# Optimization experiments

Measured on AMD Instinct MI355X. Metric: run time of the kernel, lower is better.

The kernel has to match this reference:

```python
import jax, jax.numpy as jnp
import numpy as np

# pywt db4 analysis filters (dec_lo, dec_hi), length 8
DEC_LO = np.array([-0.010597401784997278, 0.032883011666982945, 0.030841381835986965,
                   -0.18703481171888114, -0.02798376941698385, 0.6308807679295904,
                   0.7148465705525415, 0.23037781330885523], dtype=np.float32)
DEC_HI = np.array([-0.23037781330885523, 0.7148465705525415, -0.6308807679295904,
                   -0.02798376941698385, 0.18703481171888114, 0.030841381835986965,
                   -0.032883011666982945, -0.010597401784997278], dtype=np.float32)


def setup_inputs() -> dict:
    key = jax.random.key(0)
    x = jax.random.normal(key, (32, 3, 512, 512), dtype=jnp.float32)
    dec = jnp.stack([jnp.asarray(DEC_LO), jnp.asarray(DEC_HI)])  # (2, 8)
    return {"x": x, "dec": dec}


def _afb1d_last(x, dec):
    """Analysis filter bank along last axis: circular pad (end), stride-2
    cross-correlation with lo/hi filters. x: (..., L) -> (lo, hi) each (..., L//2)."""
    L = x.shape[-1]
    taps = dec.shape[-1]
    pad = taps - 1
    xp = jnp.concatenate([x, x[..., :pad]], axis=-1)          # circular pad at end
    flat = xp.reshape(-1, 1, xp.shape[-1])                    # (N, 1, L+pad)
    out = jax.lax.conv_general_dilated(
        flat, dec[:, None, :], window_strides=(2,), padding='VALID',
        dimension_numbers=('NCH', 'OIH', 'NCH'))              # (N, 2, L//2)
    out = out.reshape(*x.shape[:-1], 2, L // 2)
    return out[..., 0, :], out[..., 1, :]


def reference(x, dec):
    B, C, H, W = x.shape
    xr = x.reshape(B * C, H, W)
    # row pass (along W)
    lo_w, hi_w = _afb1d_last(xr, dec)                         # (BC, H, W//2)
    # column pass (along H): move H to last axis
    lo_t = jnp.swapaxes(lo_w, -2, -1)                         # (BC, W//2, H)
    hi_t = jnp.swapaxes(hi_w, -2, -1)
    ll, lh = _afb1d_last(lo_t, dec)                           # (BC, W//2, H//2)
    hl, hh = _afb1d_last(hi_t, dec)
    coeffs = jnp.stack([ll, lh, hl, hh], axis=1)              # (BC, 4, W//2, H//2)
    coeffs = jnp.swapaxes(coeffs, -2, -1)                     # (BC, 4, H//2, W//2)
    return coeffs.reshape(B, C * 4, H // 2, W // 2)
```

## Files before the change

### kernel.cpp

```cpp
#include <hip/hip_runtime.h>


#define TI 4
#define TJ 64
#define PR (2*TI + 6)
#define HH 512
#define WW 512

__global__ __launch_bounds__(256)
void dwt2d_db4_kernel(const float* __restrict__ x,
                      const float* __restrict__ dec,
                      float* __restrict__ out) {
    __shared__ __align__(16) float sm_lo[PR][TJ];
    __shared__ __align__(16) float sm_hi[PR][TJ];

    const int tid = threadIdx.x;

    const int n  = blockIdx.x;
    const int m  = n >> 3;
    const int jt = m & 3;
    const int it = (n & 7) * 8 + ((m >> 2) & 7);
    const int bc = m >> 5;

    const int rowBase = it * (2 * TI);
    const int colBase = jt * (2 * TJ);

    float flo[8], fhi[8];
#pragma unroll
    for (int k = 0; k < 8; ++k) { flo[k] = dec[k]; fhi[k] = dec[8 + k]; }

    const float* xb = x + (size_t)bc * HH * WW;

    for (int task = tid; task < PR * (TJ / 2); task += 256) {
        int r = task >> 5;
        int t = task & 31;
        int gr = rowBase + r;          if (gr >= HH) gr -= HH;
        int c0 = colBase + 4 * t;
        int c1 = c0 + 4;               if (c1 >= WW) c1 -= WW;
        int c2 = c0 + 8;               if (c2 >= WW) c2 -= WW;
        const float* xr = xb + gr * WW;
        float4 v0 = *(const float4*)(xr + c0);
        float4 v1 = *(const float4*)(xr + c1);
        float4 v2 = *(const float4*)(xr + c2);
        float w[12] = { v0.x, v0.y, v0.z, v0.w,
                        v1.x, v1.y, v1.z, v1.w,
                        v2.x, v2.y, v2.z, v2.w };
        float lo0 = 0.f, hi0 = 0.f, lo1 = 0.f, hi1 = 0.f;
#pragma unroll
        for (int q = 0; q < 8; ++q) {
            lo0 += w[q]     * flo[q];
            hi0 += w[q]     * fhi[q];
            lo1 += w[q + 2] * flo[q];
            hi1 += w[q + 2] * fhi[q];
        }
        *(float2*)&sm_lo[r][2 * t] = make_float2(lo0, lo1);
        *(float2*)&sm_hi[r][2 * t] = make_float2(hi0, hi1);
    }
    __syncthreads();

    {
        int i = tid >> 6;
        int j = tid & 63;
        float ll = 0.f, lh = 0.f, hl = 0.f, hh = 0.f;
#pragma unroll
        for (int p = 0; p < 8; ++p) {
            float a = sm_lo[2 * i + p][j];
            float b = sm_hi[2 * i + p][j];
            float cl = flo[p], ch = fhi[p];
            ll += a * cl; lh += a * ch;
            hl += b * cl; hh += b * ch;
        }
        int oi = it * TI + i;
        int oj = jt * TJ + j;
        size_t base = ((size_t)(bc * 4) * 256 + oi) * 256 + oj;
        __builtin_nontemporal_store(ll, &out[base]);
        __builtin_nontemporal_store(lh, &out[base + 1 * 65536]);
        __builtin_nontemporal_store(hl, &out[base + 2 * 65536]);
        __builtin_nontemporal_store(hh, &out[base + 3 * 65536]);
    }
}

extern "C" void kernel_launch(void* const* d_in, const int* in_sizes, int n_in,
                              void* d_out, int out_size, void* d_ws, size_t ws_size,
                              hipStream_t stream) {
    const float* x   = (const float*)d_in[0];
    const float* dec = (const float*)d_in[1];
    float* out = (float*)d_out;

    dim3 grid(4 * 64 * 96);
    dim3 block(256);
    dwt2d_db4_kernel<<<grid, block, 0, stream>>>(x, dec, out);
}
```

Measured before the change: 176.3 us.

## Replace shared-memory two-pass DWT with per-thread register column streaming

Result: slower. 196.6 us (+11.5%).

```diff
diff --git a/kernel.cpp b/kernel.cpp
--- a/kernel.cpp
+++ b/kernel.cpp
@@ -1,29 +1,74 @@
 #include <hip/hip_runtime.h>
 
 
-#define TI 4
-#define TJ 64
+#define TI 8
 #define PR (2*TI + 6)
 #define HH 512
 #define WW 512
+
+typedef float float4u __attribute__((ext_vector_type(4), aligned(8)));
+typedef float float2u __attribute__((ext_vector_type(2), aligned(8)));
+
+template <bool CWRAP>
+__device__ __forceinline__ void dwt_col(const float* __restrict__ xb,
+                                        int rowBase, int c0,
+                                        const float* flo, const float* fhi,
+                                        float* ll, float* lh, float* hl, float* hh) {
+#pragma unroll
+    for (int r = 0; r < PR; ++r) {
+        int gr = rowBase + r;
+        if (gr >= HH) gr -= HH;
+        const float* xr = xb + gr * WW;
+        float wv[8];
+        if constexpr (!CWRAP) {
+            float4u a = *(const float4u*)(xr + c0);
+            float4u b = *(const float4u*)(xr + c0 + 4);
+            wv[0] = a.x; wv[1] = a.y; wv[2] = a.z; wv[3] = a.w;
+            wv[4] = b.x; wv[5] = b.y; wv[6] = b.z; wv[7] = b.w;
+        } else {
+#pragma unroll
+            for (int k = 0; k < 4; ++k) {
+                int c = c0 + 2 * k;
+                if (c >= WW) c -= WW;
+                float2u v = *(const float2u*)(xr + c);
+                wv[2 * k]     = v.x;
+                wv[2 * k + 1] = v.y;
+            }
+        }
+        float rlo = 0.f, rhi = 0.f;
+#pragma unroll
+        for (int q = 0; q < 8; ++q) { rlo += wv[q] * flo[q]; rhi += wv[q] * fhi[q]; }
+#pragma unroll
+        for (int p = (r & 1); p < 8; p += 2) {
+            int d = r - p;
+            if (d >= 0 && d < 2 * TI) {
+                int i = d >> 1;
+                float cl = flo[p], ch = fhi[p];
+                ll[i] += rlo * cl; lh[i] += rlo * ch;
+                hl[i] += rhi * cl; hh[i] += rhi * ch;
+            }
+        }
+    }
+}
 
 __global__ __launch_bounds__(256)
 void dwt2d_db4_kernel(const float* __restrict__ x,
                       const float* __restrict__ dec,
                       float* __restrict__ out) {
-    __shared__ __align__(16) float sm_lo[PR][TJ];
-    __shared__ __align__(16) float sm_hi[PR][TJ];
+    const int tid  = threadIdx.x;
+    const int lane = tid & 63;
+    const int w    = tid >> 6;
 
-    const int tid = threadIdx.x;
+    const int n   = blockIdx.x;
+    const int itb = n & 7;
+    const int m   = n >> 3;
+    const int jt  = m & 3;
+    const int bc  = m >> 2;
 
-    const int n  = blockIdx.x;
-    const int m  = n >> 3;
-    const int jt = m & 3;
-    const int it = (n & 7) * 8 + ((m >> 2) & 7);
-    const int bc = m >> 5;
-
+    const int it = itb * 4 + w;
+    const int j  = jt * 64 + lane;
     const int rowBase = it * (2 * TI);
-    const int colBase = jt * (2 * TJ);
+    const int c0 = 2 * j;
 
     float flo[8], fhi[8];
 #pragma unroll
@@ -31,52 +76,20 @@
 
     const float* xb = x + (size_t)bc * HH * WW;
 
-    for (int task = tid; task < PR * (TJ / 2); task += 256) {
-        int r = task >> 5;
-        int t = task & 31;
-        int gr = rowBase + r;          if (gr >= HH) gr -= HH;
-        int c0 = colBase + 4 * t;
-        int c1 = c0 + 4;               if (c1 >= WW) c1 -= WW;
-        int c2 = c0 + 8;               if (c2 >= WW) c2 -= WW;
-        const float* xr = xb + gr * WW;
-        float4 v0 = *(const float4*)(xr + c0);
-        float4 v1 = *(const float4*)(xr + c1);
-        float4 v2 = *(const float4*)(xr + c2);
-        float w[12] = { v0.x, v0.y, v0.z, v0.w,
-                        v1.x, v1.y, v1.z, v1.w,
-                        v2.x, v2.y, v2.z, v2.w };
-        float lo0 = 0.f, hi0 = 0.f, lo1 = 0.f, hi1 = 0.f;
+    float ll[TI], lh[TI], hl[TI], hh[TI];
 #pragma unroll
-        for (int q = 0; q < 8; ++q) {
-            lo0 += w[q]     * flo[q];
-            hi0 += w[q]     * fhi[q];
-            lo1 += w[q + 2] * flo[q];
-            hi1 += w[q + 2] * fhi[q];
-        }
-        *(float2*)&sm_lo[r][2 * t] = make_float2(lo0, lo1);
-        *(float2*)&sm_hi[r][2 * t] = make_float2(hi0, hi1);
-    }
-    __syncthreads();
+    for (int i = 0; i < TI; ++i) { ll[i] = 0.f; lh[i] = 0.f; hl[i] = 0.f; hh[i] = 0.f; }
 
-    {
-        int i = tid >> 6;
-        int j = tid & 63;
-        float ll = 0.f, lh = 0.f, hl = 0.f, hh = 0.f;
+    if (jt < 3) dwt_col<false>(xb, rowBase, c0, flo, fhi, ll, lh, hl, hh);
+    else        dwt_col<true >(xb, rowBase, c0, flo, fhi, ll, lh, hl, hh);
+
+    const size_t base = ((size_t)(bc * 4) * 256 + (size_t)it * TI) * 256 + j;
 #pragma unroll
-        for (int p = 0; p < 8; ++p) {
-            float a = sm_lo[2 * i + p][j];
-            float b = sm_hi[2 * i + p][j];
-            float cl = flo[p], ch = fhi[p];
-            ll += a * cl; lh += a * ch;
-            hl += b * cl; hh += b * ch;
-        }
-        int oi = it * TI + i;
-        int oj = jt * TJ + j;
-        size_t base = ((size_t)(bc * 4) * 256 + oi) * 256 + oj;
-        __builtin_nontemporal_store(ll, &out[base]);
-        __builtin_nontemporal_store(lh, &out[base + 1 * 65536]);
-        __builtin_nontemporal_store(hl, &out[base + 2 * 65536]);
-        __builtin_nontemporal_store(hh, &out[base + 3 * 65536]);
+    for (int i = 0; i < TI; ++i) {
+        __builtin_nontemporal_store(ll[i], &out[base + (size_t)i * 256]);
+        __builtin_nontemporal_store(lh[i], &out[base + 1 * 65536 + (size_t)i * 256]);
+        __builtin_nontemporal_store(hl[i], &out[base + 2 * 65536 + (size_t)i * 256]);
+        __builtin_nontemporal_store(hh[i], &out[base + 3 * 65536 + (size_t)i * 256]);
     }
 }
 
@@ -87,7 +100,7 @@
     const float* dec = (const float*)d_in[1];
     float* out = (float*)d_out;
 
-    dim3 grid(4 * 64 * 96);
+    dim3 grid(8 * 4 * 96);
     dim3 block(256);
     dwt2d_db4_kernel<<<grid, block, 0, stream>>>(x, dec, out);
 }
```

## Widen tiles to full row width and vectorize column-pass stores per wave

Applied to the files above, without the earlier changes.

Result: slower. 185.2 us (+5.1%).

```diff
diff --git a/kernel.cpp b/kernel.cpp
--- a/kernel.cpp
+++ b/kernel.cpp
@@ -2,7 +2,6 @@
 
 
 #define TI 4
-#define TJ 64
 #define PR (2*TI + 6)
 #define HH 512
 #define WW 512
@@ -11,47 +10,48 @@
 void dwt2d_db4_kernel(const float* __restrict__ x,
                       const float* __restrict__ dec,
                       float* __restrict__ out) {
-    __shared__ __align__(16) float sm_lo[PR][TJ];
-    __shared__ __align__(16) float sm_hi[PR][TJ];
+    __shared__ __align__(16) float sm_lo[PR][256];
+    __shared__ __align__(16) float sm_hi[PR][256];
 
-    const int tid = threadIdx.x;
+    const int tid  = threadIdx.x;
+    const int w    = tid >> 6;
+    const int lane = tid & 63;
 
-    const int n  = blockIdx.x;
-    const int m  = n >> 3;
-    const int jt = m & 3;
-    const int it = (n & 7) * 8 + ((m >> 2) & 7);
-    const int bc = m >> 5;
+    const int n   = blockIdx.x;
+    const int x7  = n & 7;
+    const int k   = n >> 3;
+    const int it  = x7 * 8 + (k & 7);
+    const int bc  = k >> 3;
 
     const int rowBase = it * (2 * TI);
-    const int colBase = jt * (2 * TJ);
 
     float flo[8], fhi[8];
 #pragma unroll
-    for (int k = 0; k < 8; ++k) { flo[k] = dec[k]; fhi[k] = dec[8 + k]; }
+    for (int q = 0; q < 8; ++q) { flo[q] = dec[q]; fhi[q] = dec[8 + q]; }
 
     const float* xb = x + (size_t)bc * HH * WW;
 
-    for (int task = tid; task < PR * (TJ / 2); task += 256) {
-        int r = task >> 5;
-        int t = task & 31;
+    for (int task = tid; task < PR * 128; task += 256) {
+        int r = task >> 7;
+        int t = task & 127;
         int gr = rowBase + r;          if (gr >= HH) gr -= HH;
-        int c0 = colBase + 4 * t;
+        int c0 = 4 * t;
         int c1 = c0 + 4;               if (c1 >= WW) c1 -= WW;
         int c2 = c0 + 8;               if (c2 >= WW) c2 -= WW;
         const float* xr = xb + gr * WW;
         float4 v0 = *(const float4*)(xr + c0);
         float4 v1 = *(const float4*)(xr + c1);
         float4 v2 = *(const float4*)(xr + c2);
-        float w[12] = { v0.x, v0.y, v0.z, v0.w,
-                        v1.x, v1.y, v1.z, v1.w,
-                        v2.x, v2.y, v2.z, v2.w };
+        float wv[12] = { v0.x, v0.y, v0.z, v0.w,
+                         v1.x, v1.y, v1.z, v1.w,
+                         v2.x, v2.y, v2.z, v2.w };
         float lo0 = 0.f, hi0 = 0.f, lo1 = 0.f, hi1 = 0.f;
 #pragma unroll
         for (int q = 0; q < 8; ++q) {
-            lo0 += w[q]     * flo[q];
-            hi0 += w[q]     * fhi[q];
-            lo1 += w[q + 2] * flo[q];
-            hi1 += w[q + 2] * fhi[q];
+            lo0 += wv[q]     * flo[q];
+            hi0 += wv[q]     * fhi[q];
+            lo1 += wv[q + 2] * flo[q];
+            hi1 += wv[q + 2] * fhi[q];
         }
         *(float2*)&sm_lo[r][2 * t] = make_float2(lo0, lo1);
         *(float2*)&sm_hi[r][2 * t] = make_float2(hi0, hi1);
@@ -59,24 +59,21 @@
     __syncthreads();
 
     {
-        int i = tid >> 6;
-        int j = tid & 63;
-        float ll = 0.f, lh = 0.f, hl = 0.f, hh = 0.f;
+        const float (*src)[256] = (w >= 2) ? sm_hi : sm_lo;
+        const float* tap = (w & 1) ? fhi : flo;
+        float* op = out + (((size_t)(bc * 4 + w) * 256 + (size_t)it * TI) * 256) + 4 * lane;
 #pragma unroll
-        for (int p = 0; p < 8; ++p) {
-            float a = sm_lo[2 * i + p][j];
-            float b = sm_hi[2 * i + p][j];
-            float cl = flo[p], ch = fhi[p];
-            ll += a * cl; lh += a * ch;
-            hl += b * cl; hh += b * ch;
+        for (int i = 0; i < TI; ++i) {
+            float4 acc = make_float4(0.f, 0.f, 0.f, 0.f);
+#pragma unroll
+            for (int p = 0; p < 8; ++p) {
+                float4 v = *(const float4*)&src[2 * i + p][4 * lane];
+                float c = tap[p];
+                acc.x += v.x * c; acc.y += v.y * c;
+                acc.z += v.z * c; acc.w += v.w * c;
+            }
+            *(float4*)(op + (size_t)i * 256) = acc;
         }
-        int oi = it * TI + i;
-        int oj = jt * TJ + j;
-        size_t base = ((size_t)(bc * 4) * 256 + oi) * 256 + oj;
-        __builtin_nontemporal_store(ll, &out[base]);
-        __builtin_nontemporal_store(lh, &out[base + 1 * 65536]);
-        __builtin_nontemporal_store(hl, &out[base + 2 * 65536]);
-        __builtin_nontemporal_store(hh, &out[base + 3 * 65536]);
     }
 }
 
@@ -87,7 +84,7 @@
     const float* dec = (const float*)d_in[1];
     float* out = (float*)d_out;
 
-    dim3 grid(4 * 64 * 96);
+    dim3 grid(8 * 8 * 96);
     dim3 block(256);
     dwt2d_db4_kernel<<<grid, block, 0, stream>>>(x, dec, out);
 }
```
